# Performance work log

Measured on AMD Instinct MI355X. Metric: run time of the kernel, lower is better.

## Reference

```python
import jax, jax.numpy as jnp
import numpy as np

N = 100000
E = 1600000
F_IN, HID, N_CLS = 128, 16, 32


def setup_inputs() -> dict:
    key = jax.random.key(0)
    ks = jax.random.split(key, 10)
    x = jax.random.normal(ks[0], (N, F_IN), dtype=jnp.float32)
    edge_index = jax.random.randint(ks[1], (2, E), 0, N, dtype=jnp.int64)
    edge_weight = jax.random.uniform(ks[2], (E,), dtype=jnp.float32)
    def glorot(k, shape):
        lim = np.sqrt(6.0 / (shape[0] + shape[1])).astype(np.float32)
        return jax.random.uniform(k, shape, dtype=jnp.float32, minval=-lim, maxval=lim)
    return {
        'x': x, 'edge_index': edge_index, 'edge_weight': edge_weight,
        'W1_0': glorot(ks[3], (F_IN, HID)), 'W1_1': glorot(ks[4], (F_IN, HID)),
        'b1': jnp.zeros((HID,), jnp.float32),
        'W2_0': glorot(ks[5], (HID, N_CLS)), 'W2_1': glorot(ks[6], (HID, N_CLS)),
        'b2': jnp.zeros((N_CLS,), jnp.float32),
    }


def _cheb_conv_k2(x, row, col, edge_weight, W0, W1, b):
    # PyG ChebConv, K=2, lambda_max=2.0:
    #   T0 = x; T1 = L_hat x = D^{-1/2} A D^{-1/2} x - x
    n = x.shape[0]
    deg = jax.ops.segment_sum(edge_weight, row, num_segments=n)  # [N]
    dinv = jnp.where(deg > 0, jax.lax.rsqrt(deg), 0.0)
    norm = dinv[row] * edge_weight * dinv[col]                   # [E]
    agg = jax.ops.segment_sum(norm[:, None] * x[col], row, num_segments=n)  # [N,F]
    tx1 = agg - x
    return x @ W0 + tx1 @ W1 + b


def reference(x, edge_index, edge_weight, W1_0, W1_1, b1, W2_0, W2_1, b2):
    row, col = edge_index[0], edge_index[1]
    h = jax.nn.relu(_cheb_conv_k2(x, row, col, edge_weight, W1_0, W1_1, b1))
    # dropout(p=0) and DFA layers are identity in forward
    out = _cheb_conv_k2(h, row, col, edge_weight, W2_0, W2_1, b2)
    return jax.nn.log_softmax(out, axis=1)
```

## Files before the change

kernel.cpp:

```cpp
#include <hip/hip_runtime.h>
#include <hip/hip_bf16.h>
#include <hip/hip_fp16.h>


constexpr int NN   = 100000;
constexpr int NE   = 1600000;
constexpr int FIN  = 128;
constexpr int HID  = 16;
constexpr int NCLS = 32;

constexpr int RB    = 256;
constexpr int NBKT  = (NN + RB - 1) / RB;
constexpr int EPB   = 4096;
constexpr int EPT   = EPB / 256;
constexpr int GP    = (NE + EPB - 1) / EPB;
constexpr int CAP   = 8192;
constexpr int NTILE = NN / 16;

typedef float f32x2 __attribute__((ext_vector_type(2)));
typedef float f32x4 __attribute__((ext_vector_type(4)));
typedef short bf16x8 __attribute__((ext_vector_type(8)));

#if defined(__has_builtin)
#if __has_builtin(__builtin_amdgcn_cvt_pk_f32_fp8)
#define HAVE_CVT_FP8 1
#endif
#endif

static __device__ __forceinline__ unsigned int f2e4m3(float f) {
    union { float f; unsigned int u; } v; v.f = f;
    unsigned int s = (v.u >> 24) & 0x80u;
    unsigned int au = v.u & 0x7fffffffu;
    if (au > 0x43E00000u) au = 0x43E00000u;
    au += 0x7ffffu + ((au >> 20) & 1u);
    int e4 = (int)(au >> 23) - 120;
    unsigned int m = (au >> 20) & 7u;
    unsigned int byte = (e4 <= 0) ? 0u : (((unsigned int)e4 << 3) | m);
    return s | byte;
}
static __device__ __forceinline__ void fp8x4_fma(unsigned int v, float w, float* acc) {
#ifdef HAVE_CVT_FP8
    f32x2 lo = __builtin_amdgcn_cvt_pk_f32_fp8((int)v, false);
    f32x2 hi = __builtin_amdgcn_cvt_pk_f32_fp8((int)v, true);
    acc[0] += w * lo.x; acc[1] += w * lo.y;
    acc[2] += w * hi.x; acc[3] += w * hi.y;
#else
#pragma unroll
    for (int i = 0; i < 4; i++) {
        unsigned int b = (v >> (8 * i)) & 0xffu;
        float f = __int_as_float((int)(((b & 0x80u) << 24) | ((b & 0x7fu) << 20))) * 0x1p120f;
        acc[i] += w * f;
    }
#endif
}
static __device__ __forceinline__ unsigned short f2bf(float f) {
    union { float f; unsigned int u; } v; v.f = f;
    unsigned int r = v.u + 0x7fffu + ((v.u >> 16) & 1u);
    return (unsigned short)(r >> 16);
}
static __device__ __forceinline__ unsigned int wpack(float wf) {
    unsigned int b = __float_as_uint(wf) + 0x8000u;
    return (b >> 16) & 0x7fffu;
}
static __device__ __forceinline__ float wdec(unsigned int u) {
    return __uint_as_float((u >> 17) << 16);
}

__global__ void k_zero_cur(int* __restrict__ bucketCursor) {
    int i = blockIdx.x * blockDim.x + threadIdx.x;
    if (i < NBKT) bucketCursor[i] = 0;
}

__global__ __launch_bounds__(256) void k_partition(
    const int* __restrict__ row, const int* __restrict__ col,
    const float* __restrict__ w, int* __restrict__ bucketCursor,
    int2* __restrict__ partS) {
    __shared__ int sh_cnt[NBKT];
    __shared__ int sh_gbase[NBKT];
    __shared__ int sh_lcur[NBKT];
    int tid = threadIdx.x;
    long ebase = (long)blockIdx.x * EPB;
    int rr[EPT]; int cc[EPT]; float wv[EPT];
#pragma unroll
    for (int i = 0; i < EPT; i++) {
        long e = ebase + i * 256 + tid;
        if (e < NE) { rr[i] = row[e]; cc[i] = col[e]; wv[i] = w[e]; }
        else rr[i] = -1;
    }
    for (int i = tid; i < NBKT; i += 256) { sh_cnt[i] = 0; sh_lcur[i] = 0; }
    __syncthreads();
#pragma unroll
    for (int i = 0; i < EPT; i++)
        if (rr[i] >= 0) atomicAdd(&sh_cnt[rr[i] >> 8], 1);
    __syncthreads();
    for (int i = tid; i < NBKT; i += 256) {
        int c = sh_cnt[i];
        sh_gbase[i] = i * CAP + ((c > 0) ? atomicAdd(&bucketCursor[i], c) : 0);
    }
    __syncthreads();
#pragma unroll
    for (int i = 0; i < EPT; i++) {
        if (rr[i] >= 0) {
            int b = rr[i] >> 8;
            int pos = atomicAdd(&sh_lcur[b], 1);
            int2 v;
            v.x = cc[i] | ((rr[i] & 255) << 17);
            v.y = __float_as_int(wv[i]);
            partS[sh_gbase[b] + pos] = v;
        }
    }
}

__global__ __launch_bounds__(256) void k_bucket_sort_proj1(
    const int2* __restrict__ partS, const int* __restrict__ bucketCursor,
    unsigned int* __restrict__ partC, int* __restrict__ rowptr,
    float* __restrict__ dinv,
    const float* __restrict__ x, const float* __restrict__ W1_0,
    const float* __restrict__ W1_1, const float* __restrict__ b1,
    float* __restrict__ xa, unsigned char* __restrict__ xb8) {
    __shared__ int hist[RB];
    __shared__ int cursor[RB];
    __shared__ float dsum[RB];
    __shared__ float sh_dinv[RB];
    __shared__ int wtot[4];
    __shared__ int red[4];
    int b = blockIdx.x;
    int tid = threadIdx.x;
    int lane = tid & 63, wv = tid >> 6;
    int partial = 0;
    for (int i = tid; i < b; i += 256) partial += bucketCursor[i];
#pragma unroll
    for (int off = 1; off < 64; off <<= 1) partial += __shfl_xor(partial, off, 64);
    if (lane == 0) red[wv] = partial;
    hist[tid] = 0;
    dsum[tid] = 0.f;
    __syncthreads();
    int start = red[0] + red[1] + red[2] + red[3];
    int count = bucketCursor[b];
    const int2* src = partS + (long)b * CAP;
    for (int i = tid; i < count; i += 256)
        atomicAdd(&hist[((unsigned)src[i].x >> 17) & 255], 1);
    __syncthreads();
    int v = hist[tid];
    int sc = v;
#pragma unroll
    for (int off = 1; off < 64; off <<= 1) {
        int up = __shfl_up(sc, off, 64);
        if (lane >= off) sc += up;
    }
    if (lane == 63) wtot[wv] = sc;
    __syncthreads();
    int add = 0;
    for (int w2 = 0; w2 < wv; w2++) add += wtot[w2];
    int ex = sc + add - v;
    int node = b * RB + tid;
    if (node <= NN) rowptr[node] = start + ex;
    cursor[tid] = ex;
    __syncthreads();
    for (int i = tid; i < count; i += 256) {
        int2 p = src[i];
        int rl = ((unsigned)p.x >> 17) & 255;
        int pos = atomicAdd(&cursor[rl], 1);
        float wf = __int_as_float(p.y);
        partC[start + pos] = ((unsigned)p.x & 0x1FFFFu) | (wpack(wf) << 17);
        atomicAdd(&dsum[rl], wf);
    }
    __syncthreads();
    {
        float dsv = dsum[tid];
        float dv = dsv > 0.f ? rsqrtf(dsv) : 0.f;
        if (node < NN) dinv[node] = dv;
        sh_dinv[tid] = dv;
    }
    __syncthreads();

    {
        int pcol = lane & 15, quad = lane >> 4;
        bf16x8 bfrag[2][4];
#pragma unroll
        for (int mat = 0; mat < 2; mat++) {
            const float* W = mat ? W1_1 : W1_0;
#pragma unroll
            for (int kb = 0; kb < 4; kb++) {
                bf16x8 f;
#pragma unroll
                for (int j = 0; j < 8; j++)
                    f[j] = (short)f2bf(W[(kb * 32 + quad * 8 + j) * HID + pcol]);
                bfrag[mat][kb] = f;
            }
        }
        float b1v = b1[pcol];
#pragma unroll
        for (int i = 0; i < 4; i++) {
            int tb = wv * 4 + i;
            int wid = b * 16 + tb;
            if (wid >= NTILE) break;
            const float* xrow = x + ((long)wid * 16 + pcol) * FIN + quad * 8;
            float4 xb[8];
#pragma unroll
            for (int kb = 0; kb < 4; kb++) {
                xb[2 * kb]     = *(const float4*)(xrow + kb * 32);
                xb[2 * kb + 1] = *(const float4*)(xrow + kb * 32 + 4);
            }
            f32x4 acc0 = {0.f, 0.f, 0.f, 0.f}, acc1 = {0.f, 0.f, 0.f, 0.f};
#pragma unroll
            for (int kb = 0; kb < 4; kb++) {
                float4 a0 = xb[2 * kb], a1 = xb[2 * kb + 1];
                bf16x8 af;
                af[0] = (short)f2bf(a0.x); af[1] = (short)f2bf(a0.y);
                af[2] = (short)f2bf(a0.z); af[3] = (short)f2bf(a0.w);
                af[4] = (short)f2bf(a1.x); af[5] = (short)f2bf(a1.y);
                af[6] = (short)f2bf(a1.z); af[7] = (short)f2bf(a1.w);
                acc0 = __builtin_amdgcn_mfma_f32_16x16x32_bf16(af, bfrag[0][kb], acc0, 0, 0, 0);
                acc1 = __builtin_amdgcn_mfma_f32_16x16x32_bf16(af, bfrag[1][kb], acc1, 0, 0, 0);
            }
#pragma unroll
            for (int r = 0; r < 4; r++) {
                int lidx = tb * 16 + quad * 4 + r;
                long nd = (long)b * RB + lidx;
                float a0 = acc0[r], a1 = acc1[r];
                xa[nd * HID + pcol] = a0 - a1 + b1v;
                float dn = sh_dinv[lidx];
                xb8[nd * HID + pcol] = (unsigned char)f2e4m3(dn * a1);
            }
        }
    }
}

__global__ __launch_bounds__(256) void k_gather1(
    const int* __restrict__ rowptr, const unsigned int* __restrict__ partC,
    const float* __restrict__ dinv, const unsigned char* __restrict__ xb8,
    const float* __restrict__ xa,
    unsigned short* __restrict__ h16, unsigned char* __restrict__ h8) {
    int tile = blockIdx.x;
    int tid = threadIdx.x;
    int lane = tid & 63, wv = tid >> 6;
    int d = lane & 3, p = lane >> 2;
    int nb = tile * 16 + wv * 4;

    int s[5];
#pragma unroll
    for (int k = 0; k < 5; k++) s[k] = rowptr[nb + k];
    float4 dn4 = *(const float4*)(dinv + nb);
    float4 xav[4];
#pragma unroll
    for (int c = 0; c < 4; c++)
        xav[c] = *(const float4*)(xa + (long)(nb + c) * HID + d * 4);

    float acc[4][4];
#pragma unroll
    for (int c = 0; c < 4; c++)
#pragma unroll
        for (int i = 0; i < 4; i++) acc[c][i] = 0.f;

    int j0 = s[0] + p, j1 = s[1] + p, j2 = s[2] + p, j3 = s[3] + p;
    int e0 = s[1], e1 = s[2], e2 = s[3], e3 = s[4];
    while ((j0 < e0) | (j1 < e1) | (j2 < e2) | (j3 < e3)) {
        if (j0 < e0) {
            unsigned int u = partC[j0];
            unsigned int v = *(const unsigned int*)(xb8 + (u & 0x1FFFF) * HID + d * 4);
            fp8x4_fma(v, wdec(u), acc[0]);
            j0 += 16;
        }
        if (j1 < e1) {
            unsigned int u = partC[j1];
            unsigned int v = *(const unsigned int*)(xb8 + (u & 0x1FFFF) * HID + d * 4);
            fp8x4_fma(v, wdec(u), acc[1]);
            j1 += 16;
        }
        if (j2 < e2) {
            unsigned int u = partC[j2];
            unsigned int v = *(const unsigned int*)(xb8 + (u & 0x1FFFF) * HID + d * 4);
            fp8x4_fma(v, wdec(u), acc[2]);
            j2 += 16;
        }
        if (j3 < e3) {
            unsigned int u = partC[j3];
            unsigned int v = *(const unsigned int*)(xb8 + (u & 0x1FFFF) * HID + d * 4);
            fp8x4_fma(v, wdec(u), acc[3]);
            j3 += 16;
        }
    }
#pragma unroll
    for (int i = 0; i < 4; i++) {
#pragma unroll
        for (int c = 0; c < 4; c++) acc[c][i] += __shfl_xor(acc[c][i], 4);
#pragma unroll
        for (int c = 0; c < 4; c++) acc[c][i] += __shfl_xor(acc[c][i], 8);
#pragma unroll
        for (int c = 0; c < 4; c++) acc[c][i] += __shfl_xor(acc[c][i], 16);
#pragma unroll
        for (int c = 0; c < 4; c++) acc[c][i] += __shfl_xor(acc[c][i], 32);
    }
    if (p == 0) {
        float dnc[4] = {dn4.x, dn4.y, dn4.z, dn4.w};
#pragma unroll
        for (int c = 0; c < 4; c++) {
            long n = nb + c;
            float h0 = fmaxf(xav[c].x + dnc[c] * acc[c][0], 0.f);
            float h1 = fmaxf(xav[c].y + dnc[c] * acc[c][1], 0.f);
            float h2 = fmaxf(xav[c].z + dnc[c] * acc[c][2], 0.f);
            float h3 = fmaxf(xav[c].w + dnc[c] * acc[c][3], 0.f);
            ushort4 u;
            u.x = f2bf(h0); u.y = f2bf(h1); u.z = f2bf(h2); u.w = f2bf(h3);
            *(ushort4*)(h16 + n * HID + d * 4) = u;
            unsigned int pk = f2e4m3(dnc[c] * h0) | (f2e4m3(dnc[c] * h1) << 8)
                            | (f2e4m3(dnc[c] * h2) << 16) | (f2e4m3(dnc[c] * h3) << 24);
            *(unsigned int*)(h8 + n * HID + d * 4) = pk;
        }
    }
}

__global__ __launch_bounds__(256) void k_gather2_lsm(
    const int* __restrict__ rowptr, const unsigned int* __restrict__ partC,
    const float* __restrict__ dinv, const unsigned char* __restrict__ h8,
    const unsigned short* __restrict__ h16,
    const float* __restrict__ W2_0, const float* __restrict__ W2_1,
    const float* __restrict__ b2, float* __restrict__ out) {
    __shared__ unsigned short sh_g[16][16];
    int tile = blockIdx.x;
    int tid = threadIdx.x;
    int lane = tid & 63, wv = tid >> 6;
    int d = lane & 3, p = lane >> 2;
    int nb = tile * 16 + wv * 4;

    int s[5];
#pragma unroll
    for (int k = 0; k < 5; k++) s[k] = rowptr[nb + k];
    float4 dn4 = *(const float4*)(dinv + nb);

    float acc[4][4];
#pragma unroll
    for (int c = 0; c < 4; c++)
#pragma unroll
        for (int i = 0; i < 4; i++) acc[c][i] = 0.f;

    int j0 = s[0] + p, j1 = s[1] + p, j2 = s[2] + p, j3 = s[3] + p;
    int e0 = s[1], e1 = s[2], e2 = s[3], e3 = s[4];
    while ((j0 < e0) | (j1 < e1) | (j2 < e2) | (j3 < e3)) {
        if (j0 < e0) {
            unsigned int u = partC[j0];
            unsigned int v = *(const unsigned int*)(h8 + (u & 0x1FFFF) * HID + d * 4);
            fp8x4_fma(v, wdec(u), acc[0]);
            j0 += 16;
        }
        if (j1 < e1) {
            unsigned int u = partC[j1];
            unsigned int v = *(const unsigned int*)(h8 + (u & 0x1FFFF) * HID + d * 4);
            fp8x4_fma(v, wdec(u), acc[1]);
            j1 += 16;
        }
        if (j2 < e2) {
            unsigned int u = partC[j2];
            unsigned int v = *(const unsigned int*)(h8 + (u & 0x1FFFF) * HID + d * 4);
            fp8x4_fma(v, wdec(u), acc[2]);
            j2 += 16;
        }
        if (j3 < e3) {
            unsigned int u = partC[j3];
            unsigned int v = *(const unsigned int*)(h8 + (u & 0x1FFFF) * HID + d * 4);
            fp8x4_fma(v, wdec(u), acc[3]);
            j3 += 16;
        }
    }
#pragma unroll
    for (int i = 0; i < 4; i++) {
        acc[0][i] += __shfl_xor(acc[0][i], 4);  acc[1][i] += __shfl_xor(acc[1][i], 4);
        acc[2][i] += __shfl_xor(acc[2][i], 4);  acc[3][i] += __shfl_xor(acc[3][i], 4);
        acc[0][i] += __shfl_xor(acc[0][i], 8);  acc[1][i] += __shfl_xor(acc[1][i], 8);
        acc[2][i] += __shfl_xor(acc[2][i], 8);  acc[3][i] += __shfl_xor(acc[3][i], 8);
        acc[0][i] += __shfl_xor(acc[0][i], 16); acc[1][i] += __shfl_xor(acc[1][i], 16);
        acc[2][i] += __shfl_xor(acc[2][i], 16); acc[3][i] += __shfl_xor(acc[3][i], 16);
        acc[0][i] += __shfl_xor(acc[0][i], 32); acc[1][i] += __shfl_xor(acc[1][i], 32);
        acc[2][i] += __shfl_xor(acc[2][i], 32); acc[3][i] += __shfl_xor(acc[3][i], 32);
    }
    if (p == 0) {
        float dnc[4] = {dn4.x, dn4.y, dn4.z, dn4.w};
#pragma unroll
        for (int c = 0; c < 4; c++) {
            ushort4 u;
            u.x = f2bf(dnc[c] * acc[c][0]); u.y = f2bf(dnc[c] * acc[c][1]);
            u.z = f2bf(dnc[c] * acc[c][2]); u.w = f2bf(dnc[c] * acc[c][3]);
            *(ushort4*)&sh_g[wv * 4 + c][d * 4] = u;
        }
    }
    __syncthreads();

    if (wv == 0) {
        int pcol = lane & 15, quad = lane >> 4;
        bf16x8 bfrag[2];
#pragma unroll
        for (int c = 0; c < 2; c++) {
            bf16x8 f;
            if (quad < 2) {
#pragma unroll
                for (int j = 0; j < 8; j++) {
                    int k = quad * 8 + j;
                    f[j] = (short)f2bf(W2_0[k * NCLS + pcol + 16 * c] - W2_1[k * NCLS + pcol + 16 * c]);
                }
            } else {
#pragma unroll
                for (int j = 0; j < 8; j++) {
                    int k = (quad - 2) * 8 + j;
                    f[j] = (short)f2bf(W2_1[k * NCLS + pcol + 16 * c]);
                }
            }
            bfrag[c] = f;
        }
        bf16x8 af;
        if (quad < 2)
            af = *(const bf16x8*)(h16 + ((long)tile * 16 + pcol) * HID + (quad & 1) * 8);
        else
            af = *(const bf16x8*)&sh_g[pcol][(quad & 1) * 8];

        f32x4 c0 = {0.f, 0.f, 0.f, 0.f}, c1 = {0.f, 0.f, 0.f, 0.f};
        c0 = __builtin_amdgcn_mfma_f32_16x16x32_bf16(af, bfrag[0], c0, 0, 0, 0);
        c1 = __builtin_amdgcn_mfma_f32_16x16x32_bf16(af, bfrag[1], c1, 0, 0, 0);

        float b2a = b2[pcol], b2b = b2[pcol + 16];
#pragma unroll
        for (int r = 0; r < 4; r++) {
            long node = (long)tile * 16 + quad * 4 + r;
            float v0 = c0[r] + b2a;
            float v1 = c1[r] + b2b;
            float m = fmaxf(v0, v1);
            m = fmaxf(m, __shfl_xor(m, 1));
            m = fmaxf(m, __shfl_xor(m, 2));
            m = fmaxf(m, __shfl_xor(m, 4));
            m = fmaxf(m, __shfl_xor(m, 8));
            float sum = __expf(v0 - m) + __expf(v1 - m);
            sum += __shfl_xor(sum, 1);
            sum += __shfl_xor(sum, 2);
            sum += __shfl_xor(sum, 4);
            sum += __shfl_xor(sum, 8);
            float ls = logf(sum);
            out[node * NCLS + pcol] = v0 - m - ls;
            out[node * NCLS + pcol + 16] = v1 - m - ls;
        }
    }
}

extern "C" void kernel_launch(void* const* d_in, const int* in_sizes, int n_in,
                              void* d_out, int out_size, void* d_ws, size_t ws_size,
                              hipStream_t stream) {
    const float* x    = (const float*)d_in[0];
    const int*   ei   = (const int*)d_in[1];
    const float* ew   = (const float*)d_in[2];
    const float* W1_0 = (const float*)d_in[3];
    const float* W1_1 = (const float*)d_in[4];
    const float* b1   = (const float*)d_in[5];
    const float* W2_0 = (const float*)d_in[6];
    const float* W2_1 = (const float*)d_in[7];
    const float* b2   = (const float*)d_in[8];
    float* out = (float*)d_out;

    const int* row = ei;
    const int* col = ei + NE;

    char* ws = (char*)d_ws;
    int2*  partS     = (int2*)ws;                 ws += sizeof(int2) * (long)NBKT * CAP;
    unsigned int* partC = (unsigned int*)ws;      ws += sizeof(int) * NE;
    int*   bucketCursor = (int*)ws;               ws += sizeof(int) * NBKT;
    int*   rowptr    = (int*)ws;                  ws += sizeof(int) * (NN + 4);
    float* dinv      = (float*)ws;                ws += sizeof(float) * NN;
    float* xa        = (float*)ws;                ws += sizeof(float) * NN * HID;
    unsigned short* h16 = (unsigned short*)ws;    ws += sizeof(short) * NN * HID;
    unsigned char* xb8 = (unsigned char*)ws;      ws += sizeof(char) * NN * HID;
    unsigned char* h8  = (unsigned char*)ws;      ws += sizeof(char) * NN * HID;

    k_zero_cur<<<(NBKT + 255) / 256, 256, 0, stream>>>(bucketCursor);
    k_partition<<<GP, 256, 0, stream>>>(row, col, ew, bucketCursor, partS);
    k_bucket_sort_proj1<<<NBKT, 256, 0, stream>>>(partS, bucketCursor, partC,
                                                  rowptr, dinv, x, W1_0, W1_1,
                                                  b1, xa, xb8);
    k_gather1<<<NTILE, 256, 0, stream>>>(rowptr, partC, dinv, xb8, xa, h16, h8);
    k_gather2_lsm<<<NTILE, 256, 0, stream>>>(rowptr, partC, dinv, h8, h16,
                                             W2_0, W2_1, b2, out);
}
```

Baseline: 209.1 us.

## Replace bucket partition sort with global-atomic histogram and direct CSR scatter

Replaces the two-pass bucket partition (staging edges into fixed-capacity buckets, then sorting each bucket in shared memory) with a per-node global-atomic degree and weight-sum histogram, a prefix-scan kernel for rowptr, and a scatter kernel that places each edge directly into CSR order using per-node global atomic cursors. This drops the large intermediate partS buffer and its write and re-read. In exchange it relies on millions of contended global atomics (deg, dsum and cursor), reads the edge arrays twice, and leaves within-row edge order nondeterministic.

```diff
diff --git a/kernel.cpp b/kernel.cpp
--- a/kernel.cpp
+++ b/kernel.cpp
@@ -14,7 +14,6 @@
 constexpr int EPB   = 4096;
 constexpr int EPT   = EPB / 256;
 constexpr int GP    = (NE + EPB - 1) / EPB;
-constexpr int CAP   = 8192;
 constexpr int NTILE = NN / 16;
 
 typedef float f32x2 __attribute__((ext_vector_type(2)));
@@ -66,82 +65,60 @@
     return __uint_as_float((u >> 17) << 16);
 }
 
-__global__ void k_zero_cur(int* __restrict__ bucketCursor) {
+__global__ void k_zero(int* __restrict__ deg, float* __restrict__ dsum,
+                       int* __restrict__ btot) {
     int i = blockIdx.x * blockDim.x + threadIdx.x;
-    if (i < NBKT) bucketCursor[i] = 0;
-}
-
-__global__ __launch_bounds__(256) void k_partition(
-    const int* __restrict__ row, const int* __restrict__ col,
-    const float* __restrict__ w, int* __restrict__ bucketCursor,
-    int2* __restrict__ partS) {
-    __shared__ int sh_cnt[NBKT];
-    __shared__ int sh_gbase[NBKT];
-    __shared__ int sh_lcur[NBKT];
+    if (i < NN) { deg[i] = 0; dsum[i] = 0.f; }
+    if (i < NBKT) btot[i] = 0;
+}
+
+__global__ __launch_bounds__(256) void k_hist(
+    const int* __restrict__ row, const float* __restrict__ ew,
+    int* __restrict__ deg, float* __restrict__ dsum, int* __restrict__ btot) {
+    __shared__ int sh_bt[NBKT];
     int tid = threadIdx.x;
-    long ebase = (long)blockIdx.x * EPB;
-    int rr[EPT]; int cc[EPT]; float wv[EPT];
+    for (int i = tid; i < NBKT; i += 256) sh_bt[i] = 0;
+    __syncthreads();
+    long e0 = (long)blockIdx.x * EPB;
 #pragma unroll
     for (int i = 0; i < EPT; i++) {
-        long e = ebase + i * 256 + tid;
-        if (e < NE) { rr[i] = row[e]; cc[i] = col[e]; wv[i] = w[e]; }
-        else rr[i] = -1;
-    }
-    for (int i = tid; i < NBKT; i += 256) { sh_cnt[i] = 0; sh_lcur[i] = 0; }
-    __syncthreads();
-#pragma unroll
-    for (int i = 0; i < EPT; i++)
-        if (rr[i] >= 0) atomicAdd(&sh_cnt[rr[i] >> 8], 1);
-    __syncthreads();
-    for (int i = tid; i < NBKT; i += 256) {
-        int c = sh_cnt[i];
-        sh_gbase[i] = i * CAP + ((c > 0) ? atomicAdd(&bucketCursor[i], c) : 0);
-    }
-    __syncthreads();
-#pragma unroll
-    for (int i = 0; i < EPT; i++) {
-        if (rr[i] >= 0) {
-            int b = rr[i] >> 8;
-            int pos = atomicAdd(&sh_lcur[b], 1);
-            int2 v;
-            v.x = cc[i] | ((rr[i] & 255) << 17);
-            v.y = __float_as_int(wv[i]);
-            partS[sh_gbase[b] + pos] = v;
-        }
-    }
-}
-
-__global__ __launch_bounds__(256) void k_bucket_sort_proj1(
-    const int2* __restrict__ partS, const int* __restrict__ bucketCursor,
-    unsigned int* __restrict__ partC, int* __restrict__ rowptr,
+        long e = e0 + i * 256 + tid;
+        if (e < NE) {
+            int r = row[e];
+            float w = ew[e];
+            atomicAdd(&deg[r], 1);
+            atomicAdd(&dsum[r], w);
+            atomicAdd(&sh_bt[r >> 8], 1);
+        }
+    }
+    __syncthreads();
+    for (int i = tid; i < NBKT; i += 256)
+        if (sh_bt[i]) atomicAdd(&btot[i], sh_bt[i]);
+}
+
+__global__ __launch_bounds__(256) void k_rowptr_proj1(
+    const int* __restrict__ deg, const float* __restrict__ dsum,
+    const int* __restrict__ btot,
+    int* __restrict__ rowptr, int* __restrict__ cursor,
     float* __restrict__ dinv,
     const float* __restrict__ x, const float* __restrict__ W1_0,
     const float* __restrict__ W1_1, const float* __restrict__ b1,
     float* __restrict__ xa, unsigned char* __restrict__ xb8) {
-    __shared__ int hist[RB];
-    __shared__ int cursor[RB];
-    __shared__ float dsum[RB];
-    __shared__ float sh_dinv[RB];
     __shared__ int wtot[4];
     __shared__ int red[4];
+    __shared__ float sh_dinv[RB];
     int b = blockIdx.x;
     int tid = threadIdx.x;
     int lane = tid & 63, wv = tid >> 6;
     int partial = 0;
-    for (int i = tid; i < b; i += 256) partial += bucketCursor[i];
+    for (int i = tid; i < b; i += 256) partial += btot[i];
 #pragma unroll
     for (int off = 1; off < 64; off <<= 1) partial += __shfl_xor(partial, off, 64);
     if (lane == 0) red[wv] = partial;
-    hist[tid] = 0;
-    dsum[tid] = 0.f;
     __syncthreads();
     int start = red[0] + red[1] + red[2] + red[3];
-    int count = bucketCursor[b];
-    const int2* src = partS + (long)b * CAP;
-    for (int i = tid; i < count; i += 256)
-        atomicAdd(&hist[((unsigned)src[i].x >> 17) & 255], 1);
-    __syncthreads();
-    int v = hist[tid];
+    int node = b * RB + tid;
+    int v = (node < NN) ? deg[node] : 0;
     int sc = v;
 #pragma unroll
     for (int off = 1; off < 64; off <<= 1) {
@@ -153,24 +130,17 @@
     int add = 0;
     for (int w2 = 0; w2 < wv; w2++) add += wtot[w2];
     int ex = sc + add - v;
-    int node = b * RB + tid;
-    if (node <= NN) rowptr[node] = start + ex;
-    cursor[tid] = ex;
-    __syncthreads();
-    for (int i = tid; i < count; i += 256) {
-        int2 p = src[i];
-        int rl = ((unsigned)p.x >> 17) & 255;
-        int pos = atomicAdd(&cursor[rl], 1);
-        float wf = __int_as_float(p.y);
-        partC[start + pos] = ((unsigned)p.x & 0x1FFFFu) | (wpack(wf) << 17);
-        atomicAdd(&dsum[rl], wf);
-    }
-    __syncthreads();
-    {
-        float dsv = dsum[tid];
-        float dv = dsv > 0.f ? rsqrtf(dsv) : 0.f;
-        if (node < NN) dinv[node] = dv;
+    if (node < NN) {
+        int rp = start + ex;
+        rowptr[node] = rp;
+        cursor[node] = rp;
+        float ds = dsum[node];
+        float dv = ds > 0.f ? rsqrtf(ds) : 0.f;
+        dinv[node] = dv;
         sh_dinv[tid] = dv;
+    } else {
+        if (node == NN) rowptr[NN] = start + ex;
+        sh_dinv[tid] = 0.f;
     }
     __syncthreads();
 
@@ -223,6 +193,25 @@
                 float dn = sh_dinv[lidx];
                 xb8[nd * HID + pcol] = (unsigned char)f2e4m3(dn * a1);
             }
+        }
+    }
+}
+
+__global__ __launch_bounds__(256) void k_scatter(
+    const int* __restrict__ row, const int* __restrict__ col,
+    const float* __restrict__ ew,
+    int* __restrict__ cursor, unsigned int* __restrict__ partC) {
+    int tid = threadIdx.x;
+    long e0 = (long)blockIdx.x * EPB;
+#pragma unroll
+    for (int i = 0; i < EPT; i++) {
+        long e = e0 + i * 256 + tid;
+        if (e < NE) {
+            int r = row[e];
+            int c = col[e];
+            float w = ew[e];
+            int pos = atomicAdd(&cursor[r], 1);
+            partC[pos] = (unsigned int)c | (wpack(w) << 17);
         }
     }
 }
@@ -458,9 +447,11 @@
     const int* col = ei + NE;
 
     char* ws = (char*)d_ws;
-    int2*  partS     = (int2*)ws;                 ws += sizeof(int2) * (long)NBKT * CAP;
     unsigned int* partC = (unsigned int*)ws;      ws += sizeof(int) * NE;
-    int*   bucketCursor = (int*)ws;               ws += sizeof(int) * NBKT;
+    int*   deg       = (int*)ws;                  ws += sizeof(int) * NN;
+    int*   cursor    = (int*)ws;                  ws += sizeof(int) * NN;
+    float* dsum      = (float*)ws;                ws += sizeof(float) * NN;
+    int*   btot      = (int*)ws;                  ws += sizeof(int) * NBKT;
     int*   rowptr    = (int*)ws;                  ws += sizeof(int) * (NN + 4);
     float* dinv      = (float*)ws;                ws += sizeof(float) * NN;
     float* xa        = (float*)ws;                ws += sizeof(float) * NN * HID;
@@ -468,11 +459,11 @@
     unsigned char* xb8 = (unsigned char*)ws;      ws += sizeof(char) * NN * HID;
     unsigned char* h8  = (unsigned char*)ws;      ws += sizeof(char) * NN * HID;
 
-    k_zero_cur<<<(NBKT + 255) / 256, 256, 0, stream>>>(bucketCursor);
-    k_partition<<<GP, 256, 0, stream>>>(row, col, ew, bucketCursor, partS);
-    k_bucket_sort_proj1<<<NBKT, 256, 0, stream>>>(partS, bucketCursor, partC,
-                                                  rowptr, dinv, x, W1_0, W1_1,
-                                                  b1, xa, xb8);
+    k_zero<<<(NN + 255) / 256, 256, 0, stream>>>(deg, dsum, btot);
+    k_hist<<<GP, 256, 0, stream>>>(row, ew, deg, dsum, btot);
+    k_rowptr_proj1<<<NBKT, 256, 0, stream>>>(deg, dsum, btot, rowptr, cursor,
+                                             dinv, x, W1_0, W1_1, b1, xa, xb8);
+    k_scatter<<<GP, 256, 0, stream>>>(row, col, ew, cursor, partC);
     k_gather1<<<NTILE, 256, 0, stream>>>(rowptr, partC, dinv, xb8, xa, h16, h8);
     k_gather2_lsm<<<NTILE, 256, 0, stream>>>(rowptr, partC, dinv, h8, h16,
                                              W2_0, W2_1, b2, out);
```

After: 403.6 us. +93.0%, slower.
